# Kernel optimization log

Hardware: AMD Instinct MI355X
Metric: run time of the kernel (lower is better)

The kernel has to match this reference:

```python
import jax, jax.numpy as jnp
import numpy as np

N_EMBD = 1024
N_HEAD = 16

def setup_inputs() -> dict:
    key = jax.random.key(0)
    ks = jax.random.split(key, 6)
    C = N_EMBD
    s = 1.0 / np.sqrt(C)
    x = jax.random.normal(ks[0], (4, 2048, C), dtype=jnp.float32)
    Wk = jax.random.normal(ks[1], (C, C), dtype=jnp.float32) * s
    Wq = jax.random.normal(ks[2], (C, C), dtype=jnp.float32) * s
    Wv = jax.random.normal(ks[3], (C, C), dtype=jnp.float32) * s
    Wp = jax.random.normal(ks[4], (C, C), dtype=jnp.float32) * s
    bp = jax.random.normal(ks[5], (C,), dtype=jnp.float32) * 0.01
    return {"x": x, "Wq": Wq, "Wk": Wk, "Wv": Wv, "Wp": Wp, "bp": bp}

def reference(x, Wq, Wk, Wv, Wp, bp):
    B, T, C = x.shape
    H = N_HEAD
    d = C // H
    # projections (bias=False)
    q = (x @ Wq).reshape(B, T, H, d).transpose(0, 2, 1, 3)  # [B,H,T,d]
    k = (x @ Wk).reshape(B, T, H, d).transpose(0, 2, 1, 3)
    v = (x @ Wv).reshape(B, T, H, d).transpose(0, 2, 1, 3)
    att = jnp.einsum('bhqd,bhkd->bhqk', q, k) * (1.0 / np.sqrt(d))
    causal = jnp.tril(jnp.ones((T, T), dtype=bool))
    att = jnp.where(causal[None, None], att, jnp.float32(-jnp.inf))
    att = jax.nn.softmax(att, axis=-1)
    y = jnp.einsum('bhqk,bhkd->bhqd', att, v)  # [B,H,T,d]
    y = y.transpose(0, 2, 1, 3).reshape(B, T, C)
    return y @ Wp + bp
```

## Files before the change

### kernel.cpp

```cpp
#include <hip/hip_runtime.h>
#include <hip/hip_bf16.h>

#define N_EMBD 1024
#define N_HEADS 16
#define HD 64
#define TSEQ 2048
#define BATCH 4
#define M_TOT (BATCH*TSEQ)

typedef short s16x8 __attribute__((ext_vector_type(8)));
typedef float f32x4 __attribute__((ext_vector_type(4)));

__device__ __forceinline__ void glds16(const void* g, void* l) {
  __builtin_amdgcn_global_load_lds((const __attribute__((address_space(1))) void*)g,
                                   (__attribute__((address_space(3))) void*)l, 16, 0, 0);
}

__device__ __forceinline__ float exp_scaled(float s) {
  float r;
  asm("v_exp_f32 %0, %1\n\ts_nop 0" : "=v"(r) : "v"(s * 0.18033688011112042f));
  return r;
}

__device__ __forceinline__ unsigned cvtpk(float lo, float hi) {
  unsigned r;
  asm("v_cvt_pk_bf16_f32 %0, %1, %2" : "=v"(r) : "v"(lo), "v"(hi));
  return r;
}

__global__ __launch_bounds__(256) void xcast_kernel(const float* __restrict__ x,
                                                    __hip_bfloat16* __restrict__ xb) {
  int i = blockIdx.x * 256 + threadIdx.x;
  float4 f = ((const float4*)x)[i];
  __hip_bfloat162 p0, p1;
  p0.x = __float2bfloat16(f.x); p0.y = __float2bfloat16(f.y);
  p1.x = __float2bfloat16(f.z); p1.y = __float2bfloat16(f.w);
  ((__hip_bfloat162*)xb)[2*i]   = p0;
  ((__hip_bfloat162*)xb)[2*i+1] = p1;
}

__global__ void wcast_kernel(const float* __restrict__ Wq, const float* __restrict__ Wk,
                             const float* __restrict__ Wv, const float* __restrict__ Wp,
                             __hip_bfloat16* __restrict__ wqkvt, __hip_bfloat16* __restrict__ wpt) {
  __shared__ float tile[32][33];
  int z = blockIdx.z;
  const float* in = (z==0)?Wq:(z==1)?Wk:(z==2)?Wv:Wp;
  __hip_bfloat16* out = (z<3) ? (wqkvt + (size_t)z*N_EMBD*N_EMBD) : wpt;
  int tx = threadIdx.x, ty = threadIdx.y;
  int x  = blockIdx.x*32 + tx;
  int y0 = blockIdx.y*32;
  #pragma unroll
  for (int j=0;j<4;++j) tile[ty + j*8][tx] = in[(size_t)(y0+ty+j*8)*N_EMBD + x];
  __syncthreads();
  int xo  = y0 + tx;
  int yo0 = blockIdx.x*32;
  #pragma unroll
  for (int j=0;j<4;++j)
    out[(size_t)(yo0+ty+j*8)*N_EMBD + xo] = __float2bfloat16(tile[tx][ty+j*8]);
}

__global__ __launch_bounds__(512, 2) void gemm256_kernel(
    const __hip_bfloat16* __restrict__ A,
    const __hip_bfloat16* __restrict__ Bt,
    __hip_bfloat16* __restrict__ Qb, __hip_bfloat16* __restrict__ Kb,
    __hip_bfloat16* __restrict__ Vt) {
  __shared__ __align__(16) char smem[131072];
  int tid = threadIdx.x;
  int nb = blockIdx.x;
  int m0 = blockIdx.y * 256;
  const __hip_bfloat16* Asrc = A  + (size_t)m0 * N_EMBD;
  const __hip_bfloat16* Bsrc = Bt + (size_t)nb * 256 * N_EMBD;

  int lane = tid & 63, wv = tid >> 6, l16 = lane & 15, quad = lane >> 4;
  int swr = wv >> 2, swc = wv & 3;
  int xg = l16 & 7;
  int offc0 = ((quad    ) ^ xg) * 8;
  int offc1 = ((quad + 4) ^ xg) * 8;
  int r0  = tid >> 3;
  int gsw = ((tid & 7) ^ (r0 & 7)) * 8;
  int gln = (tid & 7) * 8;

  f32x4 acc[2][2][4][2];
  #pragma unroll
  for (int a=0;a<2;++a)
    #pragma unroll
    for (int b=0;b<2;++b)
      #pragma unroll
      for (int c=0;c<4;++c)
        #pragma unroll
        for (int d=0;d<2;++d) acc[a][b][c][d] = (f32x4){0.f,0.f,0.f,0.f};

#define STG(srcbase, kk, hh_, dst_) do {                                      \
    const __hip_bfloat16* s_ = (srcbase) + (size_t)((hh_)*128 + r0)*N_EMBD + (kk) + gsw; \
    __hip_bfloat16* d_ = (dst_) + (hh_)*8192 + r0*64 + gln;                   \
    glds16(s_, d_);                                                           \
    glds16(s_ + (size_t)64*N_EMBD, d_ + 64*64);                               \
  } while (0)
#define RDA(qm_) do { _Pragma("unroll") for (int mi=0;mi<4;++mi) {            \
    const __hip_bfloat16* p_ = Acur + ((qm_)*128 + swr*64 + mi*16 + l16)*64;  \
    af[mi][0] = *(const s16x8*)(p_ + offc0);                                  \
    af[mi][1] = *(const s16x8*)(p_ + offc1); } } while (0)
#define RDB(qn_) do { _Pragma("unroll") for (int ni=0;ni<2;++ni) {            \
    const __hip_bfloat16* p_ = Bcur + ((qn_)*128 + swc*32 + ni*16 + l16)*64;  \
    bq[ni][0] = *(const s16x8*)(p_ + offc0);                                  \
    bq[ni][1] = *(const s16x8*)(p_ + offc1); } } while (0)
#define MM(qm_,qn_) do { _Pragma("unroll") for (int mi=0;mi<4;++mi)           \
    _Pragma("unroll") for (int ni=0;ni<2;++ni) {                              \
      acc[qm_][qn_][mi][ni] = __builtin_amdgcn_mfma_f32_16x16x32_bf16(af[mi][0], bq[ni][0], acc[qm_][qn_][mi][ni],0,0,0); \
      acc[qm_][qn_][mi][ni] = __builtin_amdgcn_mfma_f32_16x16x32_bf16(af[mi][1], bq[ni][1], acc[qm_][qn_][mi][ni],0,0,0); } } while (0)

  {
    __hip_bfloat16* A0b = (__hip_bfloat16*)smem;
    __hip_bfloat16* B0b = (__hip_bfloat16*)(smem + 32768);
    STG(Asrc, 0, 0, A0b);
    STG(Bsrc, 0, 0, B0b);
    STG(Asrc, 0, 1, A0b);
    STG(Bsrc, 0, 1, B0b);
  }

  for (int t = 0; t < 16; ++t) {
    int kn = t*64 + 64;
    char* cb   = smem + (size_t)(t & 1) * 65536;
    char* nbuf = smem + (size_t)((t + 1) & 1) * 65536;
    const __hip_bfloat16* Acur = (const __hip_bfloat16*)cb;
    const __hip_bfloat16* Bcur = (const __hip_bfloat16*)(cb + 32768);
    __hip_bfloat16* An = (__hip_bfloat16*)nbuf;
    __hip_bfloat16* Bn = (__hip_bfloat16*)(nbuf + 32768);
    bool pf = (t < 15);
    s16x8 af[4][2], bq[2][2];

    if (pf) { STG(Asrc, kn, 0, An); asm volatile("s_waitcnt vmcnt(6)" ::: "memory"); }
    else    {                       asm volatile("s_waitcnt vmcnt(4)" ::: "memory"); }
    __builtin_amdgcn_s_barrier();
    __builtin_amdgcn_sched_barrier(0);
    RDA(0); RDB(0);
    asm volatile("s_waitcnt lgkmcnt(0)" ::: "memory");
    __builtin_amdgcn_sched_barrier(0);
    __builtin_amdgcn_s_setprio(1); MM(0,0); __builtin_amdgcn_s_setprio(0);

    if (pf) { STG(Bsrc, kn, 0, Bn); asm volatile("s_waitcnt vmcnt(6)" ::: "memory"); }
    else    {                       asm volatile("s_waitcnt vmcnt(2)" ::: "memory"); }
    __builtin_amdgcn_s_barrier();
    __builtin_amdgcn_sched_barrier(0);
    RDA(1);
    asm volatile("s_waitcnt lgkmcnt(0)" ::: "memory");
    __builtin_amdgcn_sched_barrier(0);
    __builtin_amdgcn_s_setprio(1); MM(1,0); __builtin_amdgcn_s_setprio(0);

    if (pf) { STG(Asrc, kn, 1, An); asm volatile("s_waitcnt vmcnt(6)" ::: "memory"); }
    else    {                       asm volatile("s_waitcnt vmcnt(0)" ::: "memory"); }
    __builtin_amdgcn_s_barrier();
    __builtin_amdgcn_sched_barrier(0);
    RDB(1);
    asm volatile("s_waitcnt lgkmcnt(0)" ::: "memory");
    __builtin_amdgcn_sched_barrier(0);
    __builtin_amdgcn_s_setprio(1); MM(1,1); __builtin_amdgcn_s_setprio(0);

    if (pf) STG(Bsrc, kn, 1, Bn);
    RDA(0);
    asm volatile("s_waitcnt lgkmcnt(0)" ::: "memory");
    __builtin_amdgcn_s_barrier();
    __builtin_amdgcn_sched_barrier(0);
    __builtin_amdgcn_s_setprio(1); MM(0,1); __builtin_amdgcn_s_setprio(0);
  }
#undef STG
#undef RDA
#undef RDB
#undef MM

  int which = nb >> 2;
  int bb = m0 >> 11, t0 = m0 & 2047;
  if (which < 2) {
    __hip_bfloat16* outp = (which==0)?Qb:Kb;
    int nloc = (nb & 3) * 256;
    #pragma unroll
    for (int qm=0;qm<2;++qm)
      #pragma unroll
      for (int qn=0;qn<2;++qn)
        #pragma unroll
        for (int mi=0;mi<4;++mi)
          #pragma unroll
          for (int ni=0;ni<2;++ni) {
            int col = nloc + qn*128 + swc*32 + ni*16 + l16;
            int hh = col >> 6, dd = col & 63;
            int trow = t0 + qm*128 + swr*64 + mi*16 + quad*4;
            __hip_bfloat16* dst = outp + ((size_t)(bb*N_HEADS + hh)*TSEQ + trow)*HD + dd;
            #pragma unroll
            for (int r=0;r<4;++r)
              dst[(size_t)r*HD] = __float2bfloat16(acc[qm][qn][mi][ni][r]);
          }
  } else {
    int hh0 = (nb & 3) * 4;
    __hip_bfloat16 (*Ts)[264] = (__hip_bfloat16(*)[264])smem;
    #pragma unroll
    for (int hd=0; hd<4; ++hd) {
      if (hd) __builtin_amdgcn_s_barrier();
      if ((swc >> 1) == (hd & 1)) {
        int qn = hd >> 1;
        int ddb = (swc & 1) * 32;
        #pragma unroll
        for (int qm=0;qm<2;++qm)
          #pragma unroll
          for (int mi=0;mi<4;++mi)
            #pragma unroll
            for (int ni=0;ni<2;++ni) {
              int dd = ddb + ni*16 + l16;
              int trow = qm*128 + swr*64 + mi*16 + quad*4;
              #pragma unroll
              for (int r=0;r<4;++r)
                Ts[dd][trow + r] = __float2bfloat16(acc[qm][qn][mi][ni][r]);
            }
      }
      __syncthreads();
      int dd = tid >> 3, tcb = (tid & 7) * 32;
      __hip_bfloat16* dst = Vt + ((size_t)(bb*N_HEADS + hh0 + hd)*HD + dd)*TSEQ + t0;
      #pragma unroll
      for (int pb=0; pb<8; ++pb) {
        int q  = tcb + pb*4;
        int pp = q & 63;
        int key = (q & 192) | (pp & 32) | ((pp & 4) << 2) | ((pp & 24) >> 1);
        *(uint2*)(dst + q) = *(const uint2*)&Ts[dd][key];
      }
    }
  }
}

__global__ __launch_bounds__(256) void gemm_kernel(
    const __hip_bfloat16* __restrict__ A,
    const __hip_bfloat16* __restrict__ Bt,
    __hip_bfloat16* __restrict__ Qb, __hip_bfloat16* __restrict__ Kb,
    __hip_bfloat16* __restrict__ Vt,
    float* __restrict__ out, const float* __restrict__ bias, int mode) {
  __shared__ __align__(16) char smem[32768];
  __hip_bfloat16* Alin = (__hip_bfloat16*)smem;
  __hip_bfloat16* Blin = (__hip_bfloat16*)(smem + 16384);
  int tid = threadIdx.x;
  int m0 = blockIdx.y*128, n0 = blockIdx.x*128;
  int w = tid>>6, lane = tid&63, l16 = lane&15, quad = lane>>4;
  int wr = w>>1, wc = w&1;
  int xg = l16 & 7;
  int off0 = ((quad    ) ^ xg)*8;
  int off1 = ((quad + 4) ^ xg)*8;
  f32x4 acc[4][4];
  #pragma unroll
  for (int mi=0;mi<4;++mi)
    #pragma unroll
    for (int ni=0;ni<4;++ni) acc[mi][ni] = (f32x4){0.f,0.f,0.f,0.f};

  for (int k0=0; k0<N_EMBD; k0+=64) {
    __syncthreads();
    #pragma unroll
    for (int rd=0; rd<4; ++rd) {
      int slot = rd*256 + tid;
      int row  = slot>>3;
      int gc8  = ((tid&7) ^ (row&7))*8;
      glds16(A  + (size_t)(m0+row)*N_EMBD + k0 + gc8, Alin + slot*8);
      glds16(Bt + (size_t)(n0+row)*N_EMBD + k0 + gc8, Blin + slot*8);
    }
    __syncthreads();
    #pragma unroll
    for (int c=0;c<2;++c) {
      int off = c ? off1 : off0;
      s16x8 af[4], bfr[4];
      #pragma unroll
      for (int mi=0;mi<4;++mi)
        af[mi] = *(const s16x8*)(Alin + (wr*64+mi*16+l16)*64 + off);
      #pragma unroll
      for (int ni=0;ni<4;++ni)
        bfr[ni] = *(const s16x8*)(Blin + (wc*64+ni*16+l16)*64 + off);
      #pragma unroll
      for (int mi=0;mi<4;++mi)
        #pragma unroll
        for (int ni=0;ni<4;++ni)
          acc[mi][ni] = __builtin_amdgcn_mfma_f32_16x16x32_bf16(af[mi], bfr[ni], acc[mi][ni],0,0,0);
    }
  }

  if (mode == 0) {
  } else {
    #pragma unroll
    for (int mi=0;mi<4;++mi) {
      #pragma unroll
      for (int ni=0;ni<4;++ni) {
        int col = n0 + wc*64 + ni*16 + l16;
        float bs = bias[col];
        #pragma unroll
        for (int r=0;r<4;++r) {
          int m = m0 + wr*64 + mi*16 + quad*4 + r;
          out[(size_t)m*N_EMBD + col] = acc[mi][ni][r] + bs;
        }
      }
    }
  }
}

__global__ __launch_bounds__(256) void attn_kernel(
    const __hip_bfloat16* __restrict__ Qb, const __hip_bfloat16* __restrict__ Kb,
    const __hip_bfloat16* __restrict__ Vt, __hip_bfloat16* __restrict__ Yb) {
  __shared__ __align__(16) __hip_bfloat16 Ks[2][64][64];
  __shared__ __align__(16) __hip_bfloat16 Vs[2][64][64];
  int tid = threadIdx.x;
  int wgid = blockIdx.x;
  int qb = (int)((0x01237564AB89CDEFull >> ((wgid>>6)*4)) & 15);
  int h  = (wgid>>2) & 15;
  int b  = wgid & 3;
  int q0 = qb*128;
  size_t bhT  = (size_t)(b*N_HEADS + h)*TSEQ;
  size_t bhHD = (size_t)(b*N_HEADS + h)*HD;
  int lane = tid&63, w = tid>>6, l16 = lane&15, quad = lane>>4;
  int wq = w*32;
  int xg = l16 & 7;
  int off0 = ((quad    ) ^ xg)*8;
  int off1 = ((quad + 4) ^ xg)*8;

  int slot0 = tid,        row0 = slot0>>3, gcA = ((tid&7) ^ (row0&7))*8;
  int slot1 = 256 + tid,  row1 = slot1>>3, gcB = ((tid&7) ^ (row1&7))*8;

  s16x8 qf[2][2];
  #pragma unroll
  for (int mi=0;mi<2;++mi) {
    const __hip_bfloat16* qrow = Qb + (bhT + q0 + wq + mi*16 + l16)*HD;
    qf[mi][0] = *(const s16x8*)(qrow + quad*8);
    qf[mi][1] = *(const s16x8*)(qrow + 32 + quad*8);
  }

  f32x4 z4 = {0.f,0.f,0.f,0.f};
  f32x4 oacc[4][2];
  #pragma unroll
  for (int nd=0;nd<4;++nd) { oacc[nd][0]=z4; oacc[nd][1]=z4; }
  float lsum[2] = {0.f, 0.f};

  int ntiles = 2*qb + 2;

  {
    glds16(Kb + (bhT + 0 + row0)*HD + gcA,    &Ks[0][0][0] + slot0*8);
    glds16(Vt + (bhHD + row0)*TSEQ + 0 + gcA, &Vs[0][0][0] + slot0*8);
    glds16(Kb + (bhT + 0 + row1)*HD + gcB,    &Ks[0][0][0] + slot1*8);
    glds16(Vt + (bhHD + row1)*TSEQ + 0 + gcB, &Vs[0][0][0] + slot1*8);
  }

  for (int t=0; t<ntiles; ++t) {
    int cur = t&1;
    int k0 = t*64;
    if (t+1 < ntiles) {
      int kn = k0 + 64;
      glds16(Kb + (bhT + kn + row0)*HD + gcA,     &Ks[cur^1][0][0] + slot0*8);
      glds16(Vt + (bhHD + row0)*TSEQ + kn + gcA,  &Vs[cur^1][0][0] + slot0*8);
      glds16(Kb + (bhT + kn + row1)*HD + gcB,     &Ks[cur^1][0][0] + slot1*8);
      glds16(Vt + (bhHD + row1)*TSEQ + kn + gcB,  &Vs[cur^1][0][0] + slot1*8);
      asm volatile("s_waitcnt vmcnt(4)" ::: "memory");
    } else {
      asm volatile("s_waitcnt vmcnt(0)" ::: "memory");
    }
    __builtin_amdgcn_s_barrier();
    __builtin_amdgcn_sched_barrier(0);

    const __hip_bfloat16* Kc = &Ks[cur][0][0];
    const __hip_bfloat16* Vc = &Vs[cur][0][0];

    f32x4 sacc[4][2];
    #pragma unroll
    for (int ni=0; ni<4; ++ni) {
      s16x8 kb0 = *(const s16x8*)(Kc + (ni*16+l16)*64 + off0);
      s16x8 kb1 = *(const s16x8*)(Kc + (ni*16+l16)*64 + off1);
      #pragma unroll
      for (int mi=0; mi<2; ++mi) {
        f32x4 s = z4;
        s = __builtin_amdgcn_mfma_f32_16x16x32_bf16(kb0, qf[mi][0], s,0,0,0);
        s = __builtin_amdgcn_mfma_f32_16x16x32_bf16(kb1, qf[mi][1], s,0,0,0);
        sacc[ni][mi] = s;
      }
    }

    unsigned pkw[2][4][2];
    if (q0 + wq >= k0 + 63) {
      #pragma unroll
      for (int ni=0; ni<4; ++ni) {
        #pragma unroll
        for (int mi=0; mi<2; ++mi) {
          float e0 = exp_scaled(sacc[ni][mi][0]);
          float e1 = exp_scaled(sacc[ni][mi][1]);
          float e2 = exp_scaled(sacc[ni][mi][2]);
          float e3 = exp_scaled(sacc[ni][mi][3]);
          lsum[mi] += (e0+e1)+(e2+e3);
          pkw[mi][ni][0] = cvtpk(e0, e1);
          pkw[mi][ni][1] = cvtpk(e2, e3);
        }
      }
    } else {
      #pragma unroll
      for (int ni=0; ni<4; ++ni) {
        int kbase = k0 + ni*16 + quad*4;
        #pragma unroll
        for (int mi=0; mi<2; ++mi) {
          int qrow = q0 + wq + mi*16 + l16;
          float e0 = (qrow >= kbase    ) ? exp_scaled(sacc[ni][mi][0]) : 0.f;
          float e1 = (qrow >= kbase + 1) ? exp_scaled(sacc[ni][mi][1]) : 0.f;
          float e2 = (qrow >= kbase + 2) ? exp_scaled(sacc[ni][mi][2]) : 0.f;
          float e3 = (qrow >= kbase + 3) ? exp_scaled(sacc[ni][mi][3]) : 0.f;
          lsum[mi] += (e0+e1)+(e2+e3);
          pkw[mi][ni][0] = cvtpk(e0, e1);
          pkw[mi][ni][1] = cvtpk(e2, e3);
        }
      }
    }

    union U8 { s16x8 v; unsigned u[4]; };
    U8 pf[2][2];
    #pragma unroll
    for (int c=0; c<2; ++c)
      #pragma unroll
      for (int mi=0; mi<2; ++mi) {
        pf[c][mi].u[0] = pkw[mi][2*c  ][0];
        pf[c][mi].u[1] = pkw[mi][2*c  ][1];
        pf[c][mi].u[2] = pkw[mi][2*c+1][0];
        pf[c][mi].u[3] = pkw[mi][2*c+1][1];
      }
    #pragma unroll
    for (int nd=0; nd<4; ++nd) {
      const __hip_bfloat16* vrow = Vc + (nd*16 + l16)*64;
      s16x8 vb0 = *(const s16x8*)(vrow + off0);
      s16x8 vb1 = *(const s16x8*)(vrow + off1);
      oacc[nd][0] = __builtin_amdgcn_mfma_f32_16x16x32_bf16(vb0, pf[0][0].v, oacc[nd][0],0,0,0);
      oacc[nd][1] = __builtin_amdgcn_mfma_f32_16x16x32_bf16(vb0, pf[0][1].v, oacc[nd][1],0,0,0);
      oacc[nd][0] = __builtin_amdgcn_mfma_f32_16x16x32_bf16(vb1, pf[1][0].v, oacc[nd][0],0,0,0);
      oacc[nd][1] = __builtin_amdgcn_mfma_f32_16x16x32_bf16(vb1, pf[1][1].v, oacc[nd][1],0,0,0);
    }

    asm volatile("s_waitcnt lgkmcnt(0)" ::: "memory");
    __builtin_amdgcn_s_barrier();
    __builtin_amdgcn_sched_barrier(0);
  }

  #pragma unroll
  for (int mi=0; mi<2; ++mi) {
    lsum[mi] += __shfl_xor(lsum[mi], 16);
    lsum[mi] += __shfl_xor(lsum[mi], 32);
  }

  #pragma unroll
  for (int mi=0; mi<2; ++mi) {
    float inv = 1.f / lsum[mi];
    int tq = q0 + wq + mi*16 + l16;
    __hip_bfloat16* yr = Yb + ((size_t)(b*TSEQ + tq))*N_EMBD + h*HD + quad*4;
    #pragma unroll
    for (int nd=0; nd<4; ++nd) {
      uint2 o;
      o.x = cvtpk(oacc[nd][mi][0]*inv, oacc[nd][mi][1]*inv);
      o.y = cvtpk(oacc[nd][mi][2]*inv, oacc[nd][mi][3]*inv);
      *(uint2*)(yr + nd*16) = o;
    }
  }
}

extern "C" void kernel_launch(void* const* d_in, const int* in_sizes, int n_in,
                              void* d_out, int out_size, void* d_ws, size_t ws_size,
                              hipStream_t stream) {
  const float* x  = (const float*)d_in[0];
  const float* Wq = (const float*)d_in[1];
  const float* Wk = (const float*)d_in[2];
  const float* Wv = (const float*)d_in[3];
  const float* Wp = (const float*)d_in[4];
  const float* bp = (const float*)d_in[5];

  char* w = (char*)d_ws;
  __hip_bfloat16* xb    = (__hip_bfloat16*)w;  w += (size_t)M_TOT*N_EMBD*2;
  __hip_bfloat16* wqkvt = (__hip_bfloat16*)w;  w += (size_t)3*N_EMBD*N_EMBD*2;
  __hip_bfloat16* wpt   = (__hip_bfloat16*)w;  w += (size_t)N_EMBD*N_EMBD*2;
  __hip_bfloat16* Qb    = (__hip_bfloat16*)w;  w += (size_t)M_TOT*N_EMBD*2;
  __hip_bfloat16* Kb    = (__hip_bfloat16*)w;  w += (size_t)M_TOT*N_EMBD*2;
  __hip_bfloat16* Vt    = (__hip_bfloat16*)w;  w += (size_t)M_TOT*N_EMBD*2;
  __hip_bfloat16* Yb    = (__hip_bfloat16*)w;

  xcast_kernel<<<dim3(M_TOT*N_EMBD/1024), dim3(256), 0, stream>>>(x, xb);
  wcast_kernel<<<dim3(32,32,4), dim3(32,8), 0, stream>>>(Wq,Wk,Wv,Wp,wqkvt,wpt);
  gemm256_kernel<<<dim3(12,32), dim3(512), 0, stream>>>(xb, wqkvt, Qb,Kb,Vt);
  attn_kernel<<<dim3(1024), dim3(256), 0, stream>>>(Qb,Kb,Vt,Yb);
  gemm_kernel<<<dim3(8,64), dim3(256), 0, stream>>>(Yb, wpt, nullptr,nullptr,nullptr,
                                                    (float*)d_out, bp, 1);
}
```

Before: 238.5 us.

## Replace four-phase interleaved GEMM schedule with single-phase contiguous warp tiles

Drops the four-quadrant ping-pong schedule inside the QKV projection GEMM. That schedule interleaved per-quadrant async global-to-LDS loads, barriers and MFMA bursts under setprio. Each k-step now issues all prefetches at once, waits once, and runs one large 8x4 MFMA block per warp over a contiguous 128x64 tile. This cuts barriers and waitcnt stalls, but needs more fragment registers and gives up the fine-grained overlap of loads with compute and the priority hints. The epilogue indexing is remapped to the new tile ownership.

Result: no change. 240.8 us (+1.0%).

```diff
diff --git a/kernel.cpp b/kernel.cpp
--- a/kernel.cpp
+++ b/kernel.cpp
@@ -80,15 +80,11 @@
   int gsw = ((tid & 7) ^ (r0 & 7)) * 8;
   int gln = (tid & 7) * 8;
 
-  f32x4 acc[2][2][4][2];
-  #pragma unroll
-  for (int a=0;a<2;++a)
-    #pragma unroll
-    for (int b=0;b<2;++b)
-      #pragma unroll
-      for (int c=0;c<4;++c)
-        #pragma unroll
-        for (int d=0;d<2;++d) acc[a][b][c][d] = (f32x4){0.f,0.f,0.f,0.f};
+  f32x4 acc[8][4];
+  #pragma unroll
+  for (int mi=0;mi<8;++mi)
+    #pragma unroll
+    for (int ni=0;ni<4;++ni) acc[mi][ni] = (f32x4){0.f,0.f,0.f,0.f};
 
 #define STG(srcbase, kk, hh_, dst_) do {                                      \
     const __hip_bfloat16* s_ = (srcbase) + (size_t)((hh_)*128 + r0)*N_EMBD + (kk) + gsw; \
@@ -96,18 +92,6 @@
     glds16(s_, d_);                                                           \
     glds16(s_ + (size_t)64*N_EMBD, d_ + 64*64);                               \
   } while (0)
-#define RDA(qm_) do { _Pragma("unroll") for (int mi=0;mi<4;++mi) {            \
-    const __hip_bfloat16* p_ = Acur + ((qm_)*128 + swr*64 + mi*16 + l16)*64;  \
-    af[mi][0] = *(const s16x8*)(p_ + offc0);                                  \
-    af[mi][1] = *(const s16x8*)(p_ + offc1); } } while (0)
-#define RDB(qn_) do { _Pragma("unroll") for (int ni=0;ni<2;++ni) {            \
-    const __hip_bfloat16* p_ = Bcur + ((qn_)*128 + swc*32 + ni*16 + l16)*64;  \
-    bq[ni][0] = *(const s16x8*)(p_ + offc0);                                  \
-    bq[ni][1] = *(const s16x8*)(p_ + offc1); } } while (0)
-#define MM(qm_,qn_) do { _Pragma("unroll") for (int mi=0;mi<4;++mi)           \
-    _Pragma("unroll") for (int ni=0;ni<2;++ni) {                              \
-      acc[qm_][qn_][mi][ni] = __builtin_amdgcn_mfma_f32_16x16x32_bf16(af[mi][0], bq[ni][0], acc[qm_][qn_][mi][ni],0,0,0); \
-      acc[qm_][qn_][mi][ni] = __builtin_amdgcn_mfma_f32_16x16x32_bf16(af[mi][1], bq[ni][1], acc[qm_][qn_][mi][ni],0,0,0); } } while (0)
 
   {
     __hip_bfloat16* A0b = (__hip_bfloat16*)smem;
@@ -126,47 +110,45 @@
     const __hip_bfloat16* Bcur = (const __hip_bfloat16*)(cb + 32768);
     __hip_bfloat16* An = (__hip_bfloat16*)nbuf;
     __hip_bfloat16* Bn = (__hip_bfloat16*)(nbuf + 32768);
-    bool pf = (t < 15);
-    s16x8 af[4][2], bq[2][2];
-
-    if (pf) { STG(Asrc, kn, 0, An); asm volatile("s_waitcnt vmcnt(6)" ::: "memory"); }
-    else    {                       asm volatile("s_waitcnt vmcnt(4)" ::: "memory"); }
+
+    if (t < 15) {
+      STG(Asrc, kn, 0, An);
+      STG(Bsrc, kn, 0, Bn);
+      STG(Asrc, kn, 1, An);
+      STG(Bsrc, kn, 1, Bn);
+      asm volatile("s_waitcnt vmcnt(8)" ::: "memory");
+    } else {
+      asm volatile("s_waitcnt vmcnt(0)" ::: "memory");
+    }
     __builtin_amdgcn_s_barrier();
     __builtin_amdgcn_sched_barrier(0);
-    RDA(0); RDB(0);
-    asm volatile("s_waitcnt lgkmcnt(0)" ::: "memory");
-    __builtin_amdgcn_sched_barrier(0);
-    __builtin_amdgcn_s_setprio(1); MM(0,0); __builtin_amdgcn_s_setprio(0);
-
-    if (pf) { STG(Bsrc, kn, 0, Bn); asm volatile("s_waitcnt vmcnt(6)" ::: "memory"); }
-    else    {                       asm volatile("s_waitcnt vmcnt(2)" ::: "memory"); }
-    __builtin_amdgcn_s_barrier();
-    __builtin_amdgcn_sched_barrier(0);
-    RDA(1);
-    asm volatile("s_waitcnt lgkmcnt(0)" ::: "memory");
-    __builtin_amdgcn_sched_barrier(0);
-    __builtin_amdgcn_s_setprio(1); MM(1,0); __builtin_amdgcn_s_setprio(0);
-
-    if (pf) { STG(Asrc, kn, 1, An); asm volatile("s_waitcnt vmcnt(6)" ::: "memory"); }
-    else    {                       asm volatile("s_waitcnt vmcnt(0)" ::: "memory"); }
-    __builtin_amdgcn_s_barrier();
-    __builtin_amdgcn_sched_barrier(0);
-    RDB(1);
-    asm volatile("s_waitcnt lgkmcnt(0)" ::: "memory");
-    __builtin_amdgcn_sched_barrier(0);
-    __builtin_amdgcn_s_setprio(1); MM(1,1); __builtin_amdgcn_s_setprio(0);
-
-    if (pf) STG(Bsrc, kn, 1, Bn);
-    RDA(0);
+
+    s16x8 af[8][2], bq[4][2];
+    #pragma unroll
+    for (int ni=0; ni<4; ++ni) {
+      const __hip_bfloat16* p_ = Bcur + (swc*64 + ni*16 + l16)*64;
+      bq[ni][0] = *(const s16x8*)(p_ + offc0);
+      bq[ni][1] = *(const s16x8*)(p_ + offc1);
+    }
+    #pragma unroll
+    for (int mi=0; mi<8; ++mi) {
+      const __hip_bfloat16* p_ = Acur + (swr*128 + mi*16 + l16)*64;
+      af[mi][0] = *(const s16x8*)(p_ + offc0);
+      af[mi][1] = *(const s16x8*)(p_ + offc1);
+    }
+    #pragma unroll
+    for (int mi=0; mi<8; ++mi)
+      #pragma unroll
+      for (int ni=0; ni<4; ++ni) {
+        acc[mi][ni] = __builtin_amdgcn_mfma_f32_16x16x32_bf16(af[mi][0], bq[ni][0], acc[mi][ni],0,0,0);
+        acc[mi][ni] = __builtin_amdgcn_mfma_f32_16x16x32_bf16(af[mi][1], bq[ni][1], acc[mi][ni],0,0,0);
+      }
+
     asm volatile("s_waitcnt lgkmcnt(0)" ::: "memory");
     __builtin_amdgcn_s_barrier();
     __builtin_amdgcn_sched_barrier(0);
-    __builtin_amdgcn_s_setprio(1); MM(0,1); __builtin_amdgcn_s_setprio(0);
   }
 #undef STG
-#undef RDA
-#undef RDB
-#undef MM
 
   int which = nb >> 2;
   int bb = m0 >> 11, t0 = m0 & 2047;
@@ -174,42 +156,34 @@
     __hip_bfloat16* outp = (which==0)?Qb:Kb;
     int nloc = (nb & 3) * 256;
     #pragma unroll
-    for (int qm=0;qm<2;++qm)
-      #pragma unroll
-      for (int qn=0;qn<2;++qn)
-        #pragma unroll
-        for (int mi=0;mi<4;++mi)
-          #pragma unroll
-          for (int ni=0;ni<2;++ni) {
-            int col = nloc + qn*128 + swc*32 + ni*16 + l16;
-            int hh = col >> 6, dd = col & 63;
-            int trow = t0 + qm*128 + swr*64 + mi*16 + quad*4;
-            __hip_bfloat16* dst = outp + ((size_t)(bb*N_HEADS + hh)*TSEQ + trow)*HD + dd;
-            #pragma unroll
-            for (int r=0;r<4;++r)
-              dst[(size_t)r*HD] = __float2bfloat16(acc[qm][qn][mi][ni][r]);
-          }
+    for (int mi=0;mi<8;++mi)
+      #pragma unroll
+      for (int ni=0;ni<4;++ni) {
+        int col = nloc + swc*64 + ni*16 + l16;
+        int hh = col >> 6, dd = col & 63;
+        int trow = t0 + swr*128 + mi*16 + quad*4;
+        __hip_bfloat16* dst = outp + ((size_t)(bb*N_HEADS + hh)*TSEQ + trow)*HD + dd;
+        #pragma unroll
+        for (int r=0;r<4;++r)
+          dst[(size_t)r*HD] = __float2bfloat16(acc[mi][ni][r]);
+      }
   } else {
     int hh0 = (nb & 3) * 4;
     __hip_bfloat16 (*Ts)[264] = (__hip_bfloat16(*)[264])smem;
     #pragma unroll
     for (int hd=0; hd<4; ++hd) {
       if (hd) __builtin_amdgcn_s_barrier();
-      if ((swc >> 1) == (hd & 1)) {
-        int qn = hd >> 1;
-        int ddb = (swc & 1) * 32;
-        #pragma unroll
-        for (int qm=0;qm<2;++qm)
+      if (swc == hd) {
+        #pragma unroll
+        for (int mi=0;mi<8;++mi)
           #pragma unroll
-          for (int mi=0;mi<4;++mi)
+          for (int ni=0;ni<4;++ni) {
+            int dd = ni*16 + l16;
+            int trow = swr*128 + mi*16 + quad*4;
             #pragma unroll
-            for (int ni=0;ni<2;++ni) {
-              int dd = ddb + ni*16 + l16;
-              int trow = qm*128 + swr*64 + mi*16 + quad*4;
-              #pragma unroll
-              for (int r=0;r<4;++r)
-                Ts[dd][trow + r] = __float2bfloat16(acc[qm][qn][mi][ni][r]);
-            }
+            for (int r=0;r<4;++r)
+              Ts[dd][trow + r] = __float2bfloat16(acc[mi][ni][r]);
+          }
       }
       __syncthreads();
       int dd = tid >> 3, tcb = (tid & 7) * 32;
```
